# Kernel optimization log

Measured on AMD Instinct MI355X. Metric: run time of the kernel, lower is better.

Reference implementation:

```python
import jax, jax.numpy as jnp
import numpy as np

N = 50000        # nodes
E = 800000       # directed edges
NUM_E = 10000    # hyperedges
NFEAT, NHID, NOUT = 256, 128, 64
K = 10
TEMP = 5.0


def gcn_prop(h, src, dst, n):
    # PyG GCNConv propagation with added self-loops: D^-1/2 (A+I) D^-1/2 h
    ew = jnp.ones(src.shape[0], h.dtype)
    deg = 1.0 + jax.ops.segment_sum(ew, dst, num_segments=n)  # self-loop adds 1
    dinv = jax.lax.rsqrt(deg)
    norm = dinv[src] * dinv[dst]                   # [E]
    out = jax.ops.segment_sum(h[src] * norm[:, None], dst, num_segments=n)
    out = out + h / deg[:, None]                   # self-loop term (weight deg^-1)
    return out


def gcn_conv(x, W, b, src, dst, n):
    return gcn_prop(x @ W, src, dst, n) + b


def hgnnp_conv(x, W, b, hv, he, n, num_e):
    # dhg HGNNPConv: theta(x) then v->e mean aggregation, then e->v mean
    h = x @ W + b
    ones = jnp.ones(hv.shape[0], h.dtype)
    e_deg = jnp.maximum(jax.ops.segment_sum(ones, he, num_segments=num_e), 1.0)
    v_deg = jnp.maximum(jax.ops.segment_sum(ones, hv, num_segments=n), 1.0)
    e_feat = jax.ops.segment_sum(h[hv], he, num_segments=num_e) / e_deg[:, None]
    v_out = jax.ops.segment_sum(e_feat[he], hv, num_segments=n) / v_deg[:, None]
    return v_out


def setup_inputs() -> dict:
    key = jax.random.key(0)
    ks = jax.random.split(key, 12)
    x = jax.random.normal(ks[0], (N, NFEAT), jnp.float32)
    edge_index = jax.random.randint(ks[1], (2, E), 0, N)
    hv_idx = jax.random.randint(ks[2], (200000,), 0, N)
    he_idx = jax.random.randint(ks[3], (200000,), 0, NUM_E)

    def glorot(k, shape):
        lim = float(np.sqrt(6.0 / (shape[0] + shape[1])))
        return jax.random.uniform(k, shape, jnp.float32, -lim, lim)

    return {
        "x": x, "edge_index": edge_index, "hv_idx": hv_idx, "he_idx": he_idx,
        "gcn_W1": glorot(ks[4], (NFEAT, NHID)), "gcn_b1": jnp.zeros((NHID,), jnp.float32),
        "gcn_W2": glorot(ks[5], (NHID, NOUT)), "gcn_b2": jnp.zeros((NOUT,), jnp.float32),
        "hg_W1": glorot(ks[6], (NFEAT, NHID)), "hg_b1": jnp.zeros((NHID,), jnp.float32),
        "hg_W2": glorot(ks[7], (NHID, NOUT)), "hg_b2": jnp.zeros((NOUT,), jnp.float32),
        "num_iter": 1,
    }


def reference(x, edge_index, hv_idx, he_idx,
              gcn_W1, gcn_b1, gcn_W2, gcn_b2,
              hg_W1, hg_b1, hg_W2, hg_b2, num_iter):
    src, dst = edge_index[0], edge_index[1]

    # HGNNP_GCN encoder (dropout is identity in eval-style reference)
    x1 = jax.nn.relu(gcn_conv(x, gcn_W1, gcn_b1, src, dst, N))
    x2 = gcn_conv(x1, gcn_W2, gcn_b2, src, dst, N)
    x3 = jax.nn.relu(hgnnp_conv(x, hg_W1, hg_b1, hv_idx, he_idx, N, NUM_E))
    x4 = hgnnp_conv(x3, hg_W2, hg_b2, hv_idx, he_idx, N, NUM_E)  # is_last: no act
    embeds = x2 * 0.5 + x4 * 0.5                     # [N, NOUT]

    # row-normalize (diag(1/||row||) @ data)
    data = embeds / jnp.linalg.norm(embeds, axis=1, keepdims=True)

    # kmeans++ init is a host-side, data-dependent pick; use deterministic
    # strided row selection from the (detached) normalized embeddings.
    init_idx = jnp.arange(K) * (N // K)
    mu = jax.lax.stop_gradient(data[init_idx])       # [K, NOUT]

    for _ in range(int(num_iter)):
        dist = data @ mu.T                           # [N, K]
        r = jax.nn.softmax(TEMP * dist, axis=1)
        cluster_r = r.sum(axis=0)                    # [K]
        cluster_mean = r.T @ data                    # [K, NOUT]
        mu = cluster_mean / cluster_r[:, None]

    dist = data @ mu.T
    r = jax.nn.softmax(TEMP * dist, axis=1)
    return mu, r, embeds, dist
```

## Files before the change

### kernel.cpp

```cpp
#include <hip/hip_runtime.h>
#include <hip/hip_bf16.h>


#define NN   50000
#define NP   50048
#define EE   800000
#define NINC 200000
#define NEH  10000
#define KCL  10
#define CBLK 782

#define MU_OFF  0
#define R_OFF   640
#define EMB_OFF 500640
#define D_OFF   3700640

typedef __hip_bfloat16 bf16;
typedef unsigned short u16;
typedef unsigned int   u32;
typedef __attribute__((ext_vector_type(8))) short short8;
typedef __attribute__((ext_vector_type(4))) float f32x4;

__device__ __forceinline__ float b2f(bf16 v){ return __bfloat162float(v); }
__device__ __forceinline__ float us2f(u16 u){ return __uint_as_float(((unsigned)u) << 16); }
__device__ __forceinline__ u16 f2bu(float f){
  unsigned u = __float_as_uint(f);
  return (u16)((u + 0x7fffu + ((u >> 16) & 1u)) >> 16);
}
__device__ __forceinline__ bf16 f2b(float f){
  u16 r = f2bu(f);
  bf16 h;
  reinterpret_cast<u16&>(h) = r;
  return h;
}
__device__ __forceinline__ float ldf(const void* p, size_t i, int isbf){
  return isbf ? b2f(((const bf16*)p)[i]) : ((const float*)p)[i];
}
__device__ __forceinline__ void stf(void* p, size_t i, float v, int isbf){
  if (isbf) ((bf16*)p)[i] = f2b(v);
  else      ((float*)p)[i] = v;
}

__global__ void k_detect(const u16* __restrict__ xr, int* flag){
  __shared__ int bad;
  if (threadIdx.x == 0) bad = 0;
  __syncthreads();
  for (int i = threadIdx.x; i < 4096; i += 256){
    int e = (xr[i] >> 7) & 0xFF;
    if (e >= 0xEF) bad = 1;
  }
  __syncthreads();
  if (threadIdx.x == 0) *flag = bad ? 0 : 1;
}

__global__ __launch_bounds__(256) void k_prep(const void* __restrict__ x, u16* __restrict__ xb,
    const void* gW1, const void* hW1, const void* gW2, const void* hW2,
    const void* gb1, const void* hb1, const void* gb2, const void* hb2,
    u16* gW1t, u16* hW1t, u16* gW2t, u16* hW2t,
    float* gb1f, float* hb1f, float* gb2f, float* hb2f,
    const int* __restrict__ flag){
  const int isbf = flag[0];
  const int blk = blockIdx.x;
  if (blk < 12500){
    int i = blk*256 + threadIdx.x;
    ushort4 o;
    if (isbf){
      o = ((const ushort4*)x)[i];
    } else {
      float4 v = ((const float4*)x)[i];
      o = make_ushort4(f2bu(v.x), f2bu(v.y), f2bu(v.z), f2bu(v.w));
    }
    ((ushort4*)xb)[i] = o;
  } else {
    int i = (blk - 12500)*256 + threadIdx.x;
    if (i < 256*128){
      int n = i >> 8, k = i & 255;
      gW1t[i] = f2bu(ldf(gW1, (size_t)k*128 + n, isbf));
      hW1t[i] = f2bu(ldf(hW1, (size_t)k*128 + n, isbf));
    }
    if (i < 64*128){
      int n = i >> 7, k = i & 127;
      gW2t[i] = f2bu(ldf(gW2, (size_t)k*64 + n, isbf));
      hW2t[i] = f2bu(ldf(hW2, (size_t)k*64 + n, isbf));
    }
    if (i < 128){ gb1f[i] = ldf(gb1,i,isbf); hb1f[i] = ldf(hb1,i,isbf); }
    if (i < 64) { gb2f[i] = ldf(gb2,i,isbf); hb2f[i] = ldf(hb2,i,isbf); }
  }
}

__global__ __launch_bounds__(256) void k_hist_all(const int* __restrict__ dstp,
    const int* __restrict__ hv, const int* __restrict__ he,
    int* HAg, int* HAv, int* HAe){
  __shared__ u32 hist[250];
  const int blk = blockIdx.x;
  const int* key; int* HA; int chunk, npb, lb;
  if (blk < 128){ key=dstp; HA=HAg; chunk=6250; npb=200; lb=blk; }
  else if (blk < 192){ key=hv; HA=HAv; chunk=3125; npb=200; lb=blk-128; }
  else { key=he; HA=HAe; chunk=3125; npb=40; lb=blk-192; }
  for (int i = threadIdx.x; i < 250; i += 256) hist[i] = 0;
  __syncthreads();
  int base = lb*chunk;
  for (int i = threadIdx.x; i < chunk; i += 256)
    atomicAdd(&hist[key[base+i]/npb], 1u);
  __syncthreads();
  int* out = HA + lb*250;
  for (int i = threadIdx.x; i < 250; i += 256) out[i] = (int)hist[i];
}

__global__ void k_scanA_all(int* HAg, int* HAv, int* HAe,
                            int* bsg, int* bsv, int* bse){
  int* HA; int* bs; int nch;
  if (blockIdx.x == 0){ HA = HAg; bs = bsg; nch = 128; }
  else if (blockIdx.x == 1){ HA = HAv; bs = bsv; nch = 64; }
  else { HA = HAe; bs = bse; nch = 64; }
  __shared__ int s[256];
  int t = threadIdx.x;
  int run = 0;
  if (t < 250){
    for (int c = 0; c < nch; ++c){
      int v = HA[c*250 + t];
      HA[c*250 + t] = run;
      run += v;
    }
  }
  int own = (t < 250) ? run : 0;
  s[t] = own; __syncthreads();
  #pragma unroll
  for (int off = 1; off < 256; off <<= 1){
    int add = (t >= off) ? s[t-off] : 0;
    __syncthreads();
    s[t] += add;
    __syncthreads();
  }
  if (t < 250) bs[t] = s[t] - own;
  if (t == 255) bs[250] = s[255];
}

__global__ __launch_bounds__(256) void k_fillA_all(const int* __restrict__ dstp,
    const int* __restrict__ srcp, const int* __restrict__ hv, const int* __restrict__ he,
    const int* HAg, const int* HAv, const int* HAe,
    const int* bsg, const int* bsv, const int* bse,
    u32* pg, u32* pv, u32* pe){
  __shared__ u32 cur[250];
  const int blk = blockIdx.x;
  const int* key; const int* val; const int* HA; const int* bs; u32* packed;
  int chunk, npb, lb;
  if (blk < 128){ key=dstp; val=srcp; HA=HAg; bs=bsg; packed=pg; chunk=6250; npb=200; lb=blk; }
  else if (blk < 192){ key=hv; val=he; HA=HAv; bs=bsv; packed=pv; chunk=3125; npb=200; lb=blk-128; }
  else { key=he; val=hv; HA=HAe; bs=bse; packed=pe; chunk=3125; npb=40; lb=blk-192; }
  const int* pre = HA + lb*250;
  for (int i = threadIdx.x; i < 250; i += 256) cur[i] = (u32)(bs[i] + pre[i]);
  __syncthreads();
  int base = lb*chunk;
  for (int i = threadIdx.x; i < chunk; i += 256){
    int k = key[base+i];
    int b = k / npb;
    u32 pos = atomicAdd(&cur[b], 1u);
    packed[pos] = ((u32)(k - b*npb) << 16) | (u32)val[base+i];
  }
}

__global__ __launch_bounds__(256) void k_fillB_all(
    const u32* pg, const u32* pv, const u32* pe,
    const int* bsg, const int* bsv, const int* bse,
    int* csr_g, int* csr_v, int* csr_e,
    int* cg, int* cv, int* ce, int* rp_g, int* rp_v, int* rp_e,
    float* dinv, float* invv, float* inve){
  __shared__ u32 hist[200];
  __shared__ int s[256];
  __shared__ u32 cur[200];
  const int blk = blockIdx.x;
  const u32* packed; const int* bs; int* csr; int* cnt; int* rp; int npb, b, mode;
  if (blk < 250){ packed=pg; bs=bsg; csr=csr_g; cnt=cg; rp=rp_g; npb=200; b=blk; mode=0; }
  else if (blk < 500){ packed=pv; bs=bsv; csr=csr_v; cnt=cv; rp=rp_v; npb=200; b=blk-250; mode=1; }
  else { packed=pe; bs=bse; csr=csr_e; cnt=ce; rp=rp_e; npb=40; b=blk-500; mode=2; }
  const int s0 = bs[b], m = bs[b+1] - s0;
  const int t = threadIdx.x;
  for (int i = t; i < npb; i += 256) hist[i] = 0;
  __syncthreads();
  for (int i = t; i < m; i += 256)
    atomicAdd(&hist[packed[s0+i] >> 16], 1u);
  __syncthreads();
  int own = (t < npb) ? (int)hist[t] : 0;
  s[t] = own; __syncthreads();
  #pragma unroll
  for (int off = 1; off < 256; off <<= 1){
    int add = (t >= off) ? s[t-off] : 0;
    __syncthreads();
    s[t] += add;
    __syncthreads();
  }
  if (t < npb){
    int excl = s[t] - own;
    int node = b*npb + t;
    cnt[node] = own;
    rp[node]  = s0 + excl;
    cur[t] = (u32)(s0 + excl);
    if (mode == 0)      dinv[node] = rsqrtf(1.0f + (float)own);
    else if (mode == 1) invv[node] = 1.0f / fmaxf((float)own, 1.0f);
    else                inve[node] = 1.0f / fmaxf((float)own, 1.0f);
  }
  if (mode == 0 && b == 249 && t < NP - NN) dinv[NN + t] = 0.f;
  __syncthreads();
  for (int i = t; i < m; i += 256){
    u32 p = packed[s0+i];
    u32 pos = atomicAdd(&cur[p >> 16], 1u);
    csr[pos] = (int)(p & 0xffffu);
  }
}

template<int KDIM, int NCOL>
__device__ __forceinline__ void gemm_body(const u16* __restrict__ A,
    const u16* __restrict__ Wt, const float* __restrict__ bias,
    const float* __restrict__ rowscale, u16* __restrict__ C, int relu, int bid)
{
  constexpr int NT  = NCOL/16;
  constexpr int LDA = 40;
  __shared__ __align__(16) u16 Asl[64][LDA];
  __shared__ __align__(16) u16 Wsl[NCOL][LDA];
  const int tid  = threadIdx.x;
  const int wave = tid >> 6, lane = tid & 63;
  const int l15 = lane & 15, l4 = lane >> 4;
  const int row0 = bid * 64;
  const int ar = tid >> 2, aq = tid & 3;
  constexpr int NW = NCOL*4/256;

  f32x4 acc[NT] = {};

  for (int kk = 0; kk < KDIM; kk += 32){
    {
      uint4 v = *(const uint4*)(A + (size_t)(row0 + ar)*KDIM + kk + aq*8);
      *(uint4*)&Asl[ar][aq*8] = v;
    }
    #pragma unroll
    for (int w2 = 0; w2 < NW; ++w2){
      int c = tid + w2*256;
      int n = c >> 2, q = c & 3;
      uint4 v = *(const uint4*)(Wt + (size_t)n*KDIM + kk + q*8);
      *(uint4*)&Wsl[n][q*8] = v;
    }
    __syncthreads();
    short8 af = *(const short8*)&Asl[wave*16 + l15][l4*8];
    #pragma unroll
    for (int t = 0; t < NT; ++t){
      short8 bf = *(const short8*)&Wsl[t*16 + l15][l4*8];
      acc[t] = __builtin_amdgcn_mfma_f32_16x16x32_bf16(af, bf, acc[t], 0, 0, 0);
    }
    __syncthreads();
  }

  #pragma unroll
  for (int t = 0; t < NT; ++t){
    int gcol = t*16 + l15;
    float b = bias ? bias[gcol] : 0.f;
    #pragma unroll
    for (int e = 0; e < 4; ++e){
      int grow = row0 + wave*16 + l4*4 + e;
      float v = acc[t][e] + b;
      if (relu) v = fmaxf(v, 0.f);
      if (rowscale) v *= rowscale[grow];
      C[(size_t)grow*NCOL + gcol] = f2bu(v);
    }
  }
}

template<int F, bool OUTBF, bool SELF>
__device__ __forceinline__ void gather_body(const int* __restrict__ rp,
    const int* __restrict__ cnt, const int* __restrict__ csr,
    const float* __restrict__ scale, const u16* __restrict__ h,
    const float* __restrict__ bias, void* __restrict__ out, int relu, int bid)
{
  const int wave = threadIdx.x >> 6, lane = threadIdx.x & 63;
  const int d = bid*4 + wave;
  const int k0 = rp[d], n = cnt[d];

  if constexpr (F == 128){
    const uint* h32 = (const uint*)h;
    float a0=0,a1=0,b0=0,b1=0,c0=0,c1=0,e0=0,e1=0;
    if (SELF){
      uint v = h32[(size_t)d*64 + lane];
      a0 = us2f((u16)v); a1 = us2f((u16)(v>>16));
    }
    for (int base = 0; base < n; base += 64){
      int mm = n - base; if (mm > 64) mm = 64;
      int idx = (lane < mm) ? csr[k0 + base + lane] : 0;
      int jj = 0;
      for (; jj + 4 <= mm; jj += 4){
        int s0=__shfl(idx,jj), s1=__shfl(idx,jj+1), s2=__shfl(idx,jj+2), s3=__shfl(idx,jj+3);
        uint v0 = h32[(size_t)s0*64 + lane];
        uint v1 = h32[(size_t)s1*64 + lane];
        uint v2 = h32[(size_t)s2*64 + lane];
        uint v3 = h32[(size_t)s3*64 + lane];
        a0 += us2f((u16)v0); a1 += us2f((u16)(v0>>16));
        b0 += us2f((u16)v1); b1 += us2f((u16)(v1>>16));
        c0 += us2f((u16)v2); c1 += us2f((u16)(v2>>16));
        e0 += us2f((u16)v3); e1 += us2f((u16)(v3>>16));
      }
      for (; jj < mm; ++jj){
        int s = __shfl(idx, jj);
        uint v = h32[(size_t)s*64 + lane];
        a0 += us2f((u16)v); a1 += us2f((u16)(v>>16));
      }
    }
    float sc = scale[d];
    float o0 = ((a0+b0)+(c0+e0))*sc;
    float o1 = ((a1+b1)+(c1+e1))*sc;
    if (bias){ o0 += bias[lane*2]; o1 += bias[lane*2+1]; }
    if (relu){ o0 = fmaxf(o0,0.f); o1 = fmaxf(o1,0.f); }
    if (OUTBF){
      ((uint*)out)[(size_t)d*64 + lane] = (uint)f2bu(o0) | ((uint)f2bu(o1) << 16);
    } else {
      ((float2*)out)[(size_t)d*64 + lane] = make_float2(o0, o1);
    }
  } else {
    float a=0,b=0,c=0,e=0;
    if (SELF) a = us2f(h[(size_t)d*64 + lane]);
    for (int base = 0; base < n; base += 64){
      int mm = n - base; if (mm > 64) mm = 64;
      int idx = (lane < mm) ? csr[k0 + base + lane] : 0;
      int jj = 0;
      for (; jj + 4 <= mm; jj += 4){
        int s0=__shfl(idx,jj), s1=__shfl(idx,jj+1), s2=__shfl(idx,jj+2), s3=__shfl(idx,jj+3);
        a += us2f(h[(size_t)s0*64 + lane]);
        b += us2f(h[(size_t)s1*64 + lane]);
        c += us2f(h[(size_t)s2*64 + lane]);
        e += us2f(h[(size_t)s3*64 + lane]);
      }
      for (; jj < mm; ++jj){
        int s = __shfl(idx, jj);
        a += us2f(h[(size_t)s*64 + lane]);
      }
    }
    float o = ((a+b)+(c+e))*scale[d];
    if (bias) o += bias[lane];
    if (relu) o = fmaxf(o, 0.f);
    if (OUTBF) ((u16*)out)[(size_t)d*64 + lane] = f2bu(o);
    else       ((float*)out)[(size_t)d*64 + lane] = o;
  }
}

__global__ __launch_bounds__(256) void k_pA(const u16* xb, const u16* gW1t,
    const float* dinv, u16* BAb){
  gemm_body<256,128>(xb, gW1t, nullptr, dinv, BAb, 0, blockIdx.x);
}
__global__ __launch_bounds__(256) void k_pB(const u16* xb, const u16* hW1t,
    const float* hb1f, u16* BEb,
    const int* rp_g, const int* cg, const int* csr_g, const float* dinv,
    const u16* BAb, const float* gb1f, u16* BBb){
  if (blockIdx.x < 782) gemm_body<256,128>(xb, hW1t, hb1f, nullptr, BEb, 0, blockIdx.x);
  else gather_body<128,true,true>(rp_g, cg, csr_g, dinv, BAb, gb1f, BBb, 1, blockIdx.x - 782);
}
__global__ __launch_bounds__(256) void k_pC(const u16* BBb, const u16* gW2t,
    const float* dinv, u16* BAb,
    const int* rp_e, const int* ce, const int* csr_e, const float* inve,
    const u16* BEb, u16* BDb){
  if (blockIdx.x < 782) gemm_body<128,64>(BBb, gW2t, nullptr, dinv, BAb, 0, blockIdx.x);
  else gather_body<128,true,false>(rp_e, ce, csr_e, inve, BEb, nullptr, BDb, 0, blockIdx.x - 782);
}
__global__ __launch_bounds__(256) void k_pD(
    const int* rp_v, const int* cv, const int* csr_v, const float* invv,
    const u16* BDb, u16* BCb,
    const int* rp_g, const int* cg, const int* csr_g, const float* dinv,
    const u16* BAb, const float* gb2f, float* x2f){
  if (blockIdx.x < 12500) gather_body<128,true,false>(rp_v, cv, csr_v, invv, BDb, nullptr, BCb, 1, blockIdx.x);
  else gather_body<64,false,true>(rp_g, cg, csr_g, dinv, BAb, gb2f, x2f, 0, blockIdx.x - 12500);
}
__global__ __launch_bounds__(256) void k_pE(const u16* BCb, const u16* hW2t,
    const float* hb2f, u16* BEb){
  gemm_body<128,64>(BCb, hW2t, hb2f, nullptr, BEb, 0, blockIdx.x);
}
__global__ __launch_bounds__(256) void k_pF(const int* rp_e, const int* ce,
    const int* csr_e, const float* inve, const u16* BEb, u16* BDb){
  gather_body<64,true,false>(rp_e, ce, csr_e, inve, BEb, nullptr, BDb, 0, blockIdx.x);
}
__global__ __launch_bounds__(256) void k_pG(const int* rp_v, const int* cv,
    const int* csr_v, const float* invv, const u16* BDb, float* x4f){
  gather_body<64,false,false>(rp_v, cv, csr_v, invv, BDb, nullptr, x4f, 0, blockIdx.x);
}

__global__ void k_embeds(const float* __restrict__ x2, const float* __restrict__ x4,
                         void* __restrict__ out, float* __restrict__ data,
                         const int* __restrict__ flag){
  int row  = blockIdx.x*4 + (threadIdx.x >> 6);
  int lane = threadIdx.x & 63;
  if (row >= NN) return;
  size_t idx = (size_t)row*64 + lane;
  float v = 0.5f*(x2[idx] + x4[idx]);
  float ss = v*v;
  #pragma unroll
  for (int off=32; off>0; off>>=1) ss += __shfl_xor(ss, off);
  float inv = rsqrtf(ss);
  data[idx] = v*inv;
  stf(out, EMB_OFF + idx, v, flag[0]);
}

__global__ void k_mu_init(const float* __restrict__ data, float* __restrict__ mu){
  int p = threadIdx.x;
  int k = p >> 6, f = p & 63;
  mu[p] = data[(size_t)k*(NN/KCL)*64 + f];
}

__global__ __launch_bounds__(640) void k_cluster_iter(const float* __restrict__ data,
    const float* __restrict__ mu, float* __restrict__ part, float* __restrict__ pcr,
    const int* __restrict__ nit, int iter)
{
  if (iter >= nit[0]) return;
  __shared__ float ms[640];
  __shared__ float dt[64][65];
  __shared__ float ds[64][11];
  const int tid = threadIdx.x;
  ms[tid] = mu[tid];
  const int base = blockIdx.x*64;
  for (int i = tid; i < 4096; i += 640){
    int r = i >> 6, f = i & 63;
    int grow = base + r;
    dt[r][f] = (grow < NN) ? data[(size_t)grow*64 + f] : 0.f;
  }
  __syncthreads();
  {
    const int row = tid & 63, k = tid >> 6;
    float dot = 0.f;
    #pragma unroll 16
    for (int f = 0; f < 64; ++f)
      dot = fmaf(dt[row][f], ms[k*64 + f], dot);
    ds[row][k] = dot;
  }
  __syncthreads();
  if (tid < 64){
    float dot[KCL];
    #pragma unroll
    for (int k = 0; k < KCL; ++k) dot[k] = ds[tid][k];
    float m = -1e30f;
    #pragma unroll
    for (int k = 0; k < KCL; ++k) m = fmaxf(m, 5.0f*dot[k]);
    float s = 0.f, ev[KCL];
    #pragma unroll
    for (int k = 0; k < KCL; ++k){ ev[k] = expf(5.0f*dot[k]-m); s += ev[k]; }
    float inv = (base + tid < NN) ? 1.0f/s : 0.f;
    #pragma unroll
    for (int k = 0; k < KCL; ++k) ds[tid][k] = ev[k]*inv;
  }
  __syncthreads();
  {
    const int f = tid & 63, k = tid >> 6;
    float acc = 0.f, crp = 0.f;
    #pragma unroll 8
    for (int t = 0; t < 64; ++t){
      float rv = ds[t][k];
      acc = fmaf(rv, dt[t][f], acc);
      crp += rv;
    }
    part[(size_t)blockIdx.x*640 + tid] = acc;
    if (f == 0) pcr[blockIdx.x*16 + k] = crp;
  }
}

__global__ void k_cred1(const float* __restrict__ part, const float* __restrict__ pcr,
                        float* __restrict__ p2, float* __restrict__ pc2,
                        const int* __restrict__ nit, int iter){
  if (iter >= nit[0]) return;
  int b = blockIdx.x, t = threadIdx.x;
  int r0 = b*20, r1 = r0 + 20; if (r1 > CBLK) r1 = CBLK;
  if (t < 640){
    float a = 0.f;
    for (int r = r0; r < r1; ++r) a += part[(size_t)r*640 + t];
    p2[(size_t)b*640 + t] = a;
  } else if (t < 640 + KCL){
    int k = t - 640;
    float a = 0.f;
    for (int r = r0; r < r1; ++r) a += pcr[r*16 + k];
    pc2[b*16 + k] = a;
  }
}

__global__ void k_cred2mu(const float* __restrict__ p2, const float* __restrict__ pc2,
                          float* __restrict__ mu, const int* __restrict__ nit, int iter){
  if (iter >= nit[0]) return;
  __shared__ float crs[16];
  int t = threadIdx.x;
  if (t >= 640 && t < 640 + KCL){
    int k = t - 640;
    float a = 0.f;
    #pragma unroll
    for (int b = 0; b < 40; ++b) a += pc2[b*16 + k];
    crs[k] = a;
  }
  __syncthreads();
  if (t < 640){
    float a = 0.f;
    #pragma unroll
    for (int b = 0; b < 40; ++b) a += p2[(size_t)b*640 + t];
    mu[t] = a / crs[t >> 6];
  }
}

__global__ __launch_bounds__(640) void k_cluster_final(const float* __restrict__ data,
    const float* __restrict__ mu, void* __restrict__ out, const int* __restrict__ flag)
{
  __shared__ float ms[640];
  __shared__ float dt[64][65];
  __shared__ float ds[64][11];
  const int tid = threadIdx.x;
  ms[tid] = mu[tid];
  const int base = blockIdx.x*64;
  for (int i = tid; i < 4096; i += 640){
    int r = i >> 6, f = i & 63;
    int grow = base + r;
    dt[r][f] = (grow < NN) ? data[(size_t)grow*64 + f] : 0.f;
  }
  __syncthreads();
  {
    const int row = tid & 63, k = tid >> 6;
    float dot = 0.f;
    #pragma unroll 16
    for (int f = 0; f < 64; ++f)
      dot = fmaf(dt[row][f], ms[k*64 + f], dot);
    ds[row][k] = dot;
  }
  __syncthreads();
  const int isbf = flag[0];
  if (blockIdx.x == 0) stf(out, MU_OFF + tid, ms[tid], isbf);
  if (tid < 64 && base + tid < NN){
    const int row = base + tid;
    float dot[KCL];
    #pragma unroll
    for (int k = 0; k < KCL; ++k) dot[k] = ds[tid][k];
    float m = -1e30f;
    #pragma unroll
    for (int k = 0; k < KCL; ++k) m = fmaxf(m, 5.0f*dot[k]);
    float s = 0.f, ev[KCL];
    #pragma unroll
    for (int k = 0; k < KCL; ++k){ ev[k] = expf(5.0f*dot[k]-m); s += ev[k]; }
    float inv = 1.0f/s;
    #pragma unroll
    for (int k = 0; k < KCL; ++k){
      stf(out, (size_t)D_OFF + (size_t)row*KCL + k, dot[k],    isbf);
      stf(out, (size_t)R_OFF + (size_t)row*KCL + k, ev[k]*inv, isbf);
    }
  }
}

extern "C" void kernel_launch(void* const* d_in, const int* in_sizes, int n_in,
                              void* d_out, int out_size, void* d_ws, size_t ws_size,
                              hipStream_t stream)
{
  const void* x   = d_in[0];
  const int*  ei  = (const int*)d_in[1];
  const int*  hv  = (const int*)d_in[2];
  const int*  he  = (const int*)d_in[3];
  const void* gW1 = d_in[4];
  const void* gb1 = d_in[5];
  const void* gW2 = d_in[6];
  const void* gb2 = d_in[7];
  const void* hW1 = d_in[8];
  const void* hb1 = d_in[9];
  const void* hW2 = d_in[10];
  const void* hb2 = d_in[11];
  const int*  nit = (const int*)d_in[12];

  float* ws = (float*)d_ws;
  size_t o = 0;
  u16*   xb  = (u16*)(ws + o); o += (size_t)NP*128;
  u16*   BAb = (u16*)(ws + o); o += (size_t)NP*64;
  u16*   BBb = (u16*)(ws + o); o += (size_t)NP*64;
  u16*   BCb = (u16*)(ws + o); o += (size_t)NP*64;
  u16*   BEb = (u16*)(ws + o); o += (size_t)NP*64;
  u16*   BDb = (u16*)(ws + o); o += (size_t)NEH*64;
  u16*  gW1t = (u16*)(ws + o); o += 16384;
  u16*  hW1t = (u16*)(ws + o); o += 16384;
  u16*  gW2t = (u16*)(ws + o); o += 4096;
  u16*  hW2t = (u16*)(ws + o); o += 4096;
  float* gb1f = ws + o; o += 128;
  float* hb1f = ws + o; o += 128;
  float* gb2f = ws + o; o += 64;
  float* hb2f = ws + o; o += 64;
  float* dinv = ws + o; o += 50048;
  float* invv = ws + o; o += 50048;
  float* inve = ws + o; o += 10048;
  float* mu   = ws + o; o += 640;
  float* part = ws + o; o += (size_t)CBLK*640;
  float* pcr  = ws + o; o += CBLK*16;
  float* p2   = ws + o; o += 40*640;
  float* pc2  = ws + o; o += 40*16;
  int*   dflg = (int*)(ws + o); o += 16;
  float* x2f   = (float*)xb;
  float* x4f   = (float*)xb + (size_t)NP*64;
  float* dataf = (float*)BBb;
  int* ib = (int*)(ws + o);
  size_t io = 0;
  int* cg    = ib + io; io += NN;
  int* cv    = ib + io; io += NN;
  int* ce    = ib + io; io += NEH + 48;
  int* rp_g  = ib + io; io += NN;
  int* rp_v  = ib + io; io += NN;
  int* rp_e  = ib + io; io += NEH + 48;
  int* csr_g = ib + io; io += EE;
  int* csr_e = ib + io; io += NINC;
  int* csr_v = ib + io; io += NINC;
  int* HAg   = ib + io; io += 128*250;
  int* HAv   = ib + io; io += 64*250;
  int* HAe   = ib + io; io += 64*250;
  int* bsg   = ib + io; io += 256;
  int* bsv   = ib + io; io += 256;
  int* bse   = ib + io; io += 256;
  u32* pg = (u32*)(ib + io); io += EE;
  u32* pv = (u32*)(ib + io); io += NINC;
  u32* pe = (u32*)(ib + io); io += NINC;

  const int* srcp = ei;
  const int* dstp = ei + EE;
  dim3 B(256);

  k_detect<<<dim3(1), B, 0, stream>>>((const u16*)x, dflg);
  k_prep<<<dim3(12628), B, 0, stream>>>(x, xb, gW1, hW1, gW2, hW2,
                                        gb1, hb1, gb2, hb2,
                                        gW1t, hW1t, gW2t, hW2t,
                                        gb1f, hb1f, gb2f, hb2f, dflg);

  k_hist_all <<<dim3(256), B, 0, stream>>>(dstp, hv, he, HAg, HAv, HAe);
  k_scanA_all<<<dim3(3),   B, 0, stream>>>(HAg, HAv, HAe, bsg, bsv, bse);
  k_fillA_all<<<dim3(256), B, 0, stream>>>(dstp, srcp, hv, he, HAg, HAv, HAe,
                                           bsg, bsv, bse, pg, pv, pe);
  k_fillB_all<<<dim3(750), B, 0, stream>>>(pg, pv, pe, bsg, bsv, bse,
                                           csr_g, csr_v, csr_e, cg, cv, ce,
                                           rp_g, rp_v, rp_e, dinv, invv, inve);

  k_pA<<<dim3(782),   B, 0, stream>>>(xb, gW1t, dinv, BAb);
  k_pB<<<dim3(13282), B, 0, stream>>>(xb, hW1t, hb1f, BEb,
                                      rp_g, cg, csr_g, dinv, BAb, gb1f, BBb);
  k_pC<<<dim3(3282),  B, 0, stream>>>(BBb, gW2t, dinv, BAb,
                                      rp_e, ce, csr_e, inve, BEb, BDb);
  k_pD<<<dim3(25000), B, 0, stream>>>(rp_v, cv, csr_v, invv, BDb, BCb,
                                      rp_g, cg, csr_g, dinv, BAb, gb2f, x2f);
  k_pE<<<dim3(782),   B, 0, stream>>>(BCb, hW2t, hb2f, BEb);
  k_pF<<<dim3(2500),  B, 0, stream>>>(rp_e, ce, csr_e, inve, BEb, BDb);
  k_pG<<<dim3(12500), B, 0, stream>>>(rp_v, cv, csr_v, invv, BDb, x4f);

  k_embeds<<<dim3((NN+3)/4), B, 0, stream>>>(x2f, x4f, d_out, dataf, dflg);

  k_mu_init<<<dim3(1), dim3(640), 0, stream>>>(dataf, mu);
  for (int it = 0; it < 4; ++it){
    k_cluster_iter<<<dim3(CBLK), dim3(640), 0, stream>>>(dataf, mu, part, pcr, nit, it);
    k_cred1       <<<dim3(40),   dim3(768), 0, stream>>>(part, pcr, p2, pc2, nit, it);
    k_cred2mu     <<<dim3(1),    dim3(768), 0, stream>>>(p2, pc2, mu, nit, it);
  }
  k_cluster_final<<<dim3(CBLK), dim3(640), 0, stream>>>(dataf, mu, d_out, dflg);
}
```

Measured before the change: 321.3 us.

## Split gather source range into passes to keep working set cache-resident

The sparse gather kernels now walk each destination's neighbour list several times. Each pass only loads source rows whose index falls in one slice of the node range (quarters for the 128-wide gathers, halves for the 64-wide ones). The goal is to shrink the set of feature rows being read at the same moment so they stay in L2/MALL instead of thrashing on random access. The cost is re-reading the CSR index list, extra shuffles and compare branches on every pass, and more divergence-free but serialized loop work per wave.

Result: slower. 446.9 us (+39.1%).

```diff
diff --git a/kernel.cpp b/kernel.cpp
--- a/kernel.cpp
+++ b/kernel.cpp
@@ -264,11 +264,12 @@
   }
 }
 
-template<int F, bool OUTBF, bool SELF>
+template<int F, bool OUTBF, bool SELF, int NPASS>
 __device__ __forceinline__ void gather_body(const int* __restrict__ rp,
     const int* __restrict__ cnt, const int* __restrict__ csr,
     const float* __restrict__ scale, const u16* __restrict__ h,
-    const float* __restrict__ bias, void* __restrict__ out, int relu, int bid)
+    const float* __restrict__ bias, void* __restrict__ out, int relu,
+    int bid, int wpass)
 {
   const int wave = threadIdx.x >> 6, lane = threadIdx.x & 63;
   const int d = bid*4 + wave;
@@ -281,25 +282,39 @@
       uint v = h32[(size_t)d*64 + lane];
       a0 = us2f((u16)v); a1 = us2f((u16)(v>>16));
     }
-    for (int base = 0; base < n; base += 64){
-      int mm = n - base; if (mm > 64) mm = 64;
-      int idx = (lane < mm) ? csr[k0 + base + lane] : 0;
-      int jj = 0;
-      for (; jj + 4 <= mm; jj += 4){
-        int s0=__shfl(idx,jj), s1=__shfl(idx,jj+1), s2=__shfl(idx,jj+2), s3=__shfl(idx,jj+3);
-        uint v0 = h32[(size_t)s0*64 + lane];
-        uint v1 = h32[(size_t)s1*64 + lane];
-        uint v2 = h32[(size_t)s2*64 + lane];
-        uint v3 = h32[(size_t)s3*64 + lane];
-        a0 += us2f((u16)v0); a1 += us2f((u16)(v0>>16));
-        b0 += us2f((u16)v1); b1 += us2f((u16)(v1>>16));
-        c0 += us2f((u16)v2); c1 += us2f((u16)(v2>>16));
-        e0 += us2f((u16)v3); e1 += us2f((u16)(v3>>16));
-      }
-      for (; jj < mm; ++jj){
-        int s = __shfl(idx, jj);
-        uint v = h32[(size_t)s*64 + lane];
-        a0 += us2f((u16)v); a1 += us2f((u16)(v>>16));
+    #pragma unroll 1
+    for (int p = 0; p < NPASS; ++p){
+      const int lo = p*wpass;
+      for (int base = 0; base < n; base += 64){
+        int mm = n - base; if (mm > 64) mm = 64;
+        int idx = (lane < mm) ? csr[k0 + base + lane] : 0;
+        int jj = 0;
+        for (; jj + 4 <= mm; jj += 4){
+          int s0=__shfl(idx,jj), s1=__shfl(idx,jj+1), s2=__shfl(idx,jj+2), s3=__shfl(idx,jj+3);
+          if (NPASS==1 || (u32)(s0-lo) < (u32)wpass){
+            uint v = h32[(size_t)s0*64 + lane];
+            a0 += us2f((u16)v); a1 += us2f((u16)(v>>16));
+          }
+          if (NPASS==1 || (u32)(s1-lo) < (u32)wpass){
+            uint v = h32[(size_t)s1*64 + lane];
+            b0 += us2f((u16)v); b1 += us2f((u16)(v>>16));
+          }
+          if (NPASS==1 || (u32)(s2-lo) < (u32)wpass){
+            uint v = h32[(size_t)s2*64 + lane];
+            c0 += us2f((u16)v); c1 += us2f((u16)(v>>16));
+          }
+          if (NPASS==1 || (u32)(s3-lo) < (u32)wpass){
+            uint v = h32[(size_t)s3*64 + lane];
+            e0 += us2f((u16)v); e1 += us2f((u16)(v>>16));
+          }
+        }
+        for (; jj < mm; ++jj){
+          int s = __shfl(idx, jj);
+          if (NPASS==1 || (u32)(s-lo) < (u32)wpass){
+            uint v = h32[(size_t)s*64 + lane];
+            a0 += us2f((u16)v); a1 += us2f((u16)(v>>16));
+          }
+        }
       }
     }
     float sc = scale[d];
@@ -315,20 +330,24 @@
   } else {
     float a=0,b=0,c=0,e=0;
     if (SELF) a = us2f(h[(size_t)d*64 + lane]);
-    for (int base = 0; base < n; base += 64){
-      int mm = n - base; if (mm > 64) mm = 64;
-      int idx = (lane < mm) ? csr[k0 + base + lane] : 0;
-      int jj = 0;
-      for (; jj + 4 <= mm; jj += 4){
-        int s0=__shfl(idx,jj), s1=__shfl(idx,jj+1), s2=__shfl(idx,jj+2), s3=__shfl(idx,jj+3);
-        a += us2f(h[(size_t)s0*64 + lane]);
-        b += us2f(h[(size_t)s1*64 + lane]);
-        c += us2f(h[(size_t)s2*64 + lane]);
-        e += us2f(h[(size_t)s3*64 + lane]);
-      }
-      for (; jj < mm; ++jj){
-        int s = __shfl(idx, jj);
-        a += us2f(h[(size_t)s*64 + lane]);
+    #pragma unroll 1
+    for (int p = 0; p < NPASS; ++p){
+      const int lo = p*wpass;
+      for (int base = 0; base < n; base += 64){
+        int mm = n - base; if (mm > 64) mm = 64;
+        int idx = (lane < mm) ? csr[k0 + base + lane] : 0;
+        int jj = 0;
+        for (; jj + 4 <= mm; jj += 4){
+          int s0=__shfl(idx,jj), s1=__shfl(idx,jj+1), s2=__shfl(idx,jj+2), s3=__shfl(idx,jj+3);
+          if (NPASS==1 || (u32)(s0-lo) < (u32)wpass) a += us2f(h[(size_t)s0*64 + lane]);
+          if (NPASS==1 || (u32)(s1-lo) < (u32)wpass) b += us2f(h[(size_t)s1*64 + lane]);
+          if (NPASS==1 || (u32)(s2-lo) < (u32)wpass) c += us2f(h[(size_t)s2*64 + lane]);
+          if (NPASS==1 || (u32)(s3-lo) < (u32)wpass) e += us2f(h[(size_t)s3*64 + lane]);
+        }
+        for (; jj < mm; ++jj){
+          int s = __shfl(idx, jj);
+          if (NPASS==1 || (u32)(s-lo) < (u32)wpass) a += us2f(h[(size_t)s*64 + lane]);
+        }
       }
     }
     float o = ((a+b)+(c+e))*scale[d];
@@ -348,22 +367,28 @@
     const int* rp_g, const int* cg, const int* csr_g, const float* dinv,
     const u16* BAb, const float* gb1f, u16* BBb){
   if (blockIdx.x < 782) gemm_body<256,128>(xb, hW1t, hb1f, nullptr, BEb, 0, blockIdx.x);
-  else gather_body<128,true,true>(rp_g, cg, csr_g, dinv, BAb, gb1f, BBb, 1, blockIdx.x - 782);
+  else gather_body<128,true,true,4>(rp_g, cg, csr_g, dinv, BAb, gb1f, BBb, 1,
+                                    blockIdx.x - 782, NP/4);
 }
 __global__ __launch_bounds__(256) void k_pC(const u16* BBb, const u16* gW2t,
     const float* dinv, u16* BAb,
     const int* rp_e, const int* ce, const int* csr_e, const float* inve,
     const u16* BEb, u16* BDb){
   if (blockIdx.x < 782) gemm_body<128,64>(BBb, gW2t, nullptr, dinv, BAb, 0, blockIdx.x);
-  else gather_body<128,true,false>(rp_e, ce, csr_e, inve, BEb, nullptr, BDb, 0, blockIdx.x - 782);
+  else gather_body<128,true,false,4>(rp_e, ce, csr_e, inve, BEb, nullptr, BDb, 0,
+                                     blockIdx.x - 782, NP/4);
 }
 __global__ __launch_bounds__(256) void k_pD(
     const int* rp_v, const int* cv, const int* csr_v, const float* invv,
     const u16* BDb, u16* BCb,
     const int* rp_g, const int* cg, const int* csr_g, const float* dinv,
     const u16* BAb, const float* gb2f, float* x2f){
-  if (blockIdx.x < 12500) gather_body<128,true,false>(rp_v, cv, csr_v, invv, BDb, nullptr, BCb, 1, blockIdx.x);
-  else gather_body<64,false,true>(rp_g, cg, csr_g, dinv, BAb, gb2f, x2f, 0, blockIdx.x - 12500);
+  if (blockIdx.x < 12500)
+    gather_body<128,true,false,1>(rp_v, cv, csr_v, invv, BDb, nullptr, BCb, 1,
+                                  blockIdx.x, NEH);
+  else
+    gather_body<64,false,true,2>(rp_g, cg, csr_g, dinv, BAb, gb2f, x2f, 0,
+                                 blockIdx.x - 12500, NP/2);
 }
 __global__ __launch_bounds__(256) void k_pE(const u16* BCb, const u16* hW2t,
     const float* hb2f, u16* BEb){
@@ -371,11 +396,13 @@
 }
 __global__ __launch_bounds__(256) void k_pF(const int* rp_e, const int* ce,
     const int* csr_e, const float* inve, const u16* BEb, u16* BDb){
-  gather_body<64,true,false>(rp_e, ce, csr_e, inve, BEb, nullptr, BDb, 0, blockIdx.x);
+  gather_body<64,true,false,2>(rp_e, ce, csr_e, inve, BEb, nullptr, BDb, 0,
+                               blockIdx.x, NP/2);
 }
 __global__ __launch_bounds__(256) void k_pG(const int* rp_v, const int* cv,
     const int* csr_v, const float* invv, const u16* BDb, float* x4f){
-  gather_body<64,false,false>(rp_v, cv, csr_v, invv, BDb, nullptr, x4f, 0, blockIdx.x);
+  gather_body<64,false,false,1>(rp_v, cv, csr_v, invv, BDb, nullptr, x4f, 0,
+                                blockIdx.x, NEH);
 }
 
 __global__ void k_embeds(const float* __restrict__ x2, const float* __restrict__ x4,
```
